# Performance work log

Measured on AMD Instinct MI355X. Metric: run time of the kernel, lower is better.

## Reference

```python
import jax, jax.numpy as jnp
import numpy as np

B = 2048      # query positions
N_OBS = 2048  # observed star positions
P = 15        # poly features = (d_max+1)(d_max+2)/2, d_max=4
G = 21        # graph features
E = 64        # n_graph_elems (columns of graph_dic)
D = 256       # opd_dim


def setup_inputs() -> dict:
    key = jax.random.key(0)
    k1, k2, k3, k4, k5, k6 = jax.random.split(key, 6)
    positions = jax.random.uniform(k1, (B, 2), dtype=jnp.float32)
    obs_pos = jax.random.uniform(k2, (N_OBS, 2), dtype=jnp.float32)
    poly_dic = jax.random.normal(k3, (N_OBS, P), dtype=jnp.float32)
    graph_dic = jax.random.normal(k4, (N_OBS, E), dtype=jnp.float32)
    alpha_poly = jnp.eye(P, dtype=jnp.float32)
    alpha_graph = jnp.eye(E, G, dtype=jnp.float32)
    S_poly = jax.random.uniform(k5, (P, D, D), minval=-0.001, maxval=0.001, dtype=jnp.float32)
    S_graph = jax.random.uniform(k6, (G, D, D), minval=-0.001, maxval=0.001, dtype=jnp.float32)
    return {"positions": positions, "obs_pos": obs_pos, "poly_dic": poly_dic,
            "graph_dic": graph_dic, "alpha_poly": alpha_poly, "alpha_graph": alpha_graph,
            "S_poly": S_poly, "S_graph": S_graph}


def reference(positions, obs_pos, poly_dic, graph_dic, alpha_poly, alpha_graph, S_poly, S_graph):
    # Brute-force 1-NN: [B, N_obs] squared distances, argmin over obs axis.
    d2 = jnp.sum((positions[:, None, :] - obs_pos[None, :, :]) ** 2, axis=-1)
    indices = jnp.argmin(d2, axis=1)                    # [B] int
    # Gather dictionary rows, mix with small alpha matrices.
    a_poly = poly_dic[indices] @ alpha_poly             # [B, P]
    a_graph = graph_dic[indices] @ alpha_graph          # [B, G]
    # Small-rank expansion into dense OPD maps.
    opd = (jnp.einsum('bp,pij->bij', a_poly, S_poly)
           + jnp.einsum('bg,gij->bij', a_graph, S_graph))  # [B, D, D]
    return opd
```

## Files before the change

kernel.cpp:

```cpp
#include <hip/hip_runtime.h>

#define NB 2048
#define NOBS 2048
#define NP 15
#define NG 21
#define NE 64
#define ND 256
#define NK 36
#define NDD (ND*ND)
#define RB 16
#define CT 4

typedef float vfloat4 __attribute__((ext_vector_type(4)));

__global__ __launch_bounds__(256) void knn_coeff_kernel(
    const float* __restrict__ positions,
    const float* __restrict__ obs_pos,
    const float* __restrict__ poly_dic,
    const float* __restrict__ graph_dic,
    const float* __restrict__ alpha_poly,
    const float* __restrict__ alpha_graph,
    float* __restrict__ coeffT)
{
    __shared__ float2 sobs[NOBS];
    __shared__ float  sd[256];
    __shared__ int    si[256];
    __shared__ int    sidx;

    const int tid = threadIdx.x;
    const int b   = blockIdx.x;

    const float2* obs2 = (const float2*)obs_pos;
    for (int i = tid; i < NOBS; i += 256) sobs[i] = obs2[i];

    const float qx = positions[2*b + 0];
    const float qy = positions[2*b + 1];
    __syncthreads();

    float bestd = 3.4e38f;
    int   besti = 0;
    #pragma unroll
    for (int it = 0; it < NOBS/256; ++it) {
        const int i = tid + it*256;
        const float dx = qx - sobs[i].x;
        const float dy = qy - sobs[i].y;
        const float d2 = dx*dx + dy*dy;
        if (d2 < bestd) { bestd = d2; besti = i; }
    }
    sd[tid] = bestd; si[tid] = besti;
    __syncthreads();

    for (int s = 128; s > 0; s >>= 1) {
        if (tid < s) {
            const float d2 = sd[tid + s];
            const int   i2 = si[tid + s];
            if (d2 < sd[tid] || (d2 == sd[tid] && i2 < si[tid])) {
                sd[tid] = d2; si[tid] = i2;
            }
        }
        __syncthreads();
    }
    if (tid == 0) sidx = si[0];
    __syncthreads();
    const int idx = sidx;

    if (tid < NP) {
        float acc = 0.f;
        #pragma unroll
        for (int q = 0; q < NP; ++q)
            acc += poly_dic[idx*NP + q] * alpha_poly[q*NP + tid];
        coeffT[(size_t)tid*NB + b] = acc;
    } else if (tid < NK) {
        const int g = tid - NP;
        float acc = 0.f;
        #pragma unroll
        for (int e = 0; e < NE; ++e)
            acc += graph_dic[idx*NE + e] * alpha_graph[e*NG + g];
        coeffT[(size_t)tid*NB + b] = acc;
    }
}

__global__ __launch_bounds__(256) void expand_kernel(
    const float* __restrict__ coeffT,
    const float* __restrict__ S_poly,
    const float* __restrict__ S_graph,
    float* __restrict__ out)
{
    const int j  = (blockIdx.x * 256 + threadIdx.x) * CT;
    const int b0 = blockIdx.y * RB;

    float acc[RB][CT];
    #pragma unroll
    for (int r = 0; r < RB; ++r)
        #pragma unroll
        for (int c = 0; c < CT; ++c)
            acc[r][c] = 0.f;

    #pragma unroll 2
    for (int k = 0; k < NP; ++k) {
        const vfloat4 sv = *(const vfloat4*)(S_poly + (size_t)k*NDD + j);
        const float*  cr = coeffT + (size_t)k*NB + b0;
        float cv[RB];
        *(vfloat4*)&cv[0]  = *(const vfloat4*)(cr + 0);
        *(vfloat4*)&cv[4]  = *(const vfloat4*)(cr + 4);
        *(vfloat4*)&cv[8]  = *(const vfloat4*)(cr + 8);
        *(vfloat4*)&cv[12] = *(const vfloat4*)(cr + 12);
        #pragma unroll
        for (int r = 0; r < RB; ++r)
            #pragma unroll
            for (int c = 0; c < CT; ++c)
                acc[r][c] += cv[r] * sv[c];
    }

    #pragma unroll 2
    for (int k = 0; k < NG; ++k) {
        const vfloat4 sv = *(const vfloat4*)(S_graph + (size_t)k*NDD + j);
        const float*  cr = coeffT + (size_t)(NP + k)*NB + b0;
        float cv[RB];
        *(vfloat4*)&cv[0]  = *(const vfloat4*)(cr + 0);
        *(vfloat4*)&cv[4]  = *(const vfloat4*)(cr + 4);
        *(vfloat4*)&cv[8]  = *(const vfloat4*)(cr + 8);
        *(vfloat4*)&cv[12] = *(const vfloat4*)(cr + 12);
        #pragma unroll
        for (int r = 0; r < RB; ++r)
            #pragma unroll
            for (int c = 0; c < CT; ++c)
                acc[r][c] += cv[r] * sv[c];
    }

    #pragma unroll
    for (int r = 0; r < RB; ++r) {
        vfloat4 v;
        v.x = acc[r][0]; v.y = acc[r][1]; v.z = acc[r][2]; v.w = acc[r][3];
        __builtin_nontemporal_store(
            v, (vfloat4*)(out + (size_t)(b0 + r)*NDD + j));
    }
}

extern "C" void kernel_launch(void* const* d_in, const int* in_sizes, int n_in,
                              void* d_out, int out_size, void* d_ws, size_t ws_size,
                              hipStream_t stream) {
    const float* positions   = (const float*)d_in[0];
    const float* obs_pos     = (const float*)d_in[1];
    const float* poly_dic    = (const float*)d_in[2];
    const float* graph_dic   = (const float*)d_in[3];
    const float* alpha_poly  = (const float*)d_in[4];
    const float* alpha_graph = (const float*)d_in[5];
    const float* S_poly      = (const float*)d_in[6];
    const float* S_graph     = (const float*)d_in[7];
    float* out = (float*)d_out;

    float* coeffT = (float*)d_ws;

    knn_coeff_kernel<<<NB, 256, 0, stream>>>(
        positions, obs_pos, poly_dic, graph_dic, alpha_poly, alpha_graph, coeffT);

    dim3 grid2(NDD/(256*CT), NB/RB);
    expand_kernel<<<grid2, 256, 0, stream>>>(coeffT, S_poly, S_graph, out);
}
```

Baseline: 613.4 us.

## Batch 8 queries per kNN block with shuffle argmin; merge expand loops with prefetch

```diff
diff --git a/kernel.cpp b/kernel.cpp
--- a/kernel.cpp
+++ b/kernel.cpp
@@ -10,6 +10,7 @@
 #define NDD (ND*ND)
 #define RB 16
 #define CT 4
+#define QB 8
 
 typedef float vfloat4 __attribute__((ext_vector_type(4)));
 
@@ -23,60 +24,63 @@
     float* __restrict__ coeffT)
 {
     __shared__ float2 sobs[NOBS];
-    __shared__ float  sd[256];
-    __shared__ int    si[256];
-    __shared__ int    sidx;
+    __shared__ float  sap[NP*NP];
+    __shared__ float  sag[NE*NG];
+    __shared__ int    sbest[QB];
 
     const int tid = threadIdx.x;
-    const int b   = blockIdx.x;
 
     const float2* obs2 = (const float2*)obs_pos;
     for (int i = tid; i < NOBS; i += 256) sobs[i] = obs2[i];
-
-    const float qx = positions[2*b + 0];
-    const float qy = positions[2*b + 1];
+    for (int i = tid; i < NP*NP; i += 256) sap[i] = alpha_poly[i];
+    for (int i = tid; i < NE*NG; i += 256) sag[i] = alpha_graph[i];
     __syncthreads();
 
-    float bestd = 3.4e38f;
-    int   besti = 0;
-    #pragma unroll
-    for (int it = 0; it < NOBS/256; ++it) {
-        const int i = tid + it*256;
+    const int w    = tid >> 6;
+    const int lane = tid & 63;
+    const int half = lane >> 5;
+    const int l32  = lane & 31;
+    const int q    = blockIdx.x * QB + 2*w + half;
+
+    const float qx = positions[2*q + 0];
+    const float qy = positions[2*q + 1];
+
+    unsigned long long best = ~0ull;
+    #pragma unroll 8
+    for (int it = 0; it < NOBS/32; ++it) {
+        const int i = l32 + it*32;
         const float dx = qx - sobs[i].x;
         const float dy = qy - sobs[i].y;
         const float d2 = dx*dx + dy*dy;
-        if (d2 < bestd) { bestd = d2; besti = i; }
+        const unsigned long long key =
+            ((unsigned long long)__float_as_uint(d2) << 32) | (unsigned)i;
+        if (key < best) best = key;
     }
-    sd[tid] = bestd; si[tid] = besti;
+    #pragma unroll
+    for (int m = 16; m > 0; m >>= 1) {
+        const unsigned long long o = __shfl_xor(best, m, 32);
+        if (o < best) best = o;
+    }
+    if (l32 == 0) sbest[2*w + half] = (int)(best & 0xffffffffu);
     __syncthreads();
 
-    for (int s = 128; s > 0; s >>= 1) {
-        if (tid < s) {
-            const float d2 = sd[tid + s];
-            const int   i2 = si[tid + s];
-            if (d2 < sd[tid] || (d2 == sd[tid] && i2 < si[tid])) {
-                sd[tid] = d2; si[tid] = i2;
-            }
+    for (int t = tid; t < QB*NK; t += 256) {
+        const int qq  = t / NK;
+        const int k   = t - qq*NK;
+        const int idx = sbest[qq];
+        const int b   = blockIdx.x * QB + qq;
+        float acc = 0.f;
+        if (k < NP) {
+            #pragma unroll
+            for (int p = 0; p < NP; ++p)
+                acc += poly_dic[idx*NP + p] * sap[p*NP + k];
+        } else {
+            const int g = k - NP;
+            #pragma unroll
+            for (int e = 0; e < NE; ++e)
+                acc += graph_dic[idx*NE + e] * sag[e*NG + g];
         }
-        __syncthreads();
-    }
-    if (tid == 0) sidx = si[0];
-    __syncthreads();
-    const int idx = sidx;
-
-    if (tid < NP) {
-        float acc = 0.f;
-        #pragma unroll
-        for (int q = 0; q < NP; ++q)
-            acc += poly_dic[idx*NP + q] * alpha_poly[q*NP + tid];
-        coeffT[(size_t)tid*NB + b] = acc;
-    } else if (tid < NK) {
-        const int g = tid - NP;
-        float acc = 0.f;
-        #pragma unroll
-        for (int e = 0; e < NE; ++e)
-            acc += graph_dic[idx*NE + e] * alpha_graph[e*NG + g];
-        coeffT[(size_t)tid*NB + b] = acc;
+        coeffT[(size_t)k*NB + b] = acc;
     }
 }
 
@@ -89,51 +93,44 @@
     const int j  = (blockIdx.x * 256 + threadIdx.x) * CT;
     const int b0 = blockIdx.y * RB;
 
-    float acc[RB][CT];
+    const float* __restrict__ sp = S_poly  + j;
+    const float* __restrict__ sg = S_graph + j;
+    const float* __restrict__ cb = coeffT + b0;
+
+    vfloat4 acc[RB];
     #pragma unroll
-    for (int r = 0; r < RB; ++r)
+    for (int r = 0; r < RB; ++r) acc[r] = (vfloat4)0.f;
+
+    vfloat4 sv = *(const vfloat4*)sp;
+    #pragma unroll
+    for (int k = 0; k < NK; ++k) {
+        vfloat4 svn = sv;
+        if (k + 1 < NK) {
+            const float* nsrc = (k + 1 < NP)
+                ? (sp + (size_t)(k + 1) * NDD)
+                : (sg + (size_t)(k + 1 - NP) * NDD);
+            svn = *(const vfloat4*)nsrc;
+        }
+        const float* cr = cb + (size_t)k * NB;
+        vfloat4 c0 = *(const vfloat4*)(cr + 0);
+        vfloat4 c1 = *(const vfloat4*)(cr + 4);
+        vfloat4 c2 = *(const vfloat4*)(cr + 8);
+        vfloat4 c3 = *(const vfloat4*)(cr + 12);
         #pragma unroll
-        for (int c = 0; c < CT; ++c)
-            acc[r][c] = 0.f;
-
-    #pragma unroll 2
-    for (int k = 0; k < NP; ++k) {
-        const vfloat4 sv = *(const vfloat4*)(S_poly + (size_t)k*NDD + j);
-        const float*  cr = coeffT + (size_t)k*NB + b0;
-        float cv[RB];
-        *(vfloat4*)&cv[0]  = *(const vfloat4*)(cr + 0);
-        *(vfloat4*)&cv[4]  = *(const vfloat4*)(cr + 4);
-        *(vfloat4*)&cv[8]  = *(const vfloat4*)(cr + 8);
-        *(vfloat4*)&cv[12] = *(const vfloat4*)(cr + 12);
+        for (int r = 0; r < 4; ++r) acc[r     ] += c0[r] * sv;
         #pragma unroll
-        for (int r = 0; r < RB; ++r)
-            #pragma unroll
-            for (int c = 0; c < CT; ++c)
-                acc[r][c] += cv[r] * sv[c];
-    }
-
-    #pragma unroll 2
-    for (int k = 0; k < NG; ++k) {
-        const vfloat4 sv = *(const vfloat4*)(S_graph + (size_t)k*NDD + j);
-        const float*  cr = coeffT + (size_t)(NP + k)*NB + b0;
-        float cv[RB];
-        *(vfloat4*)&cv[0]  = *(const vfloat4*)(cr + 0);
-        *(vfloat4*)&cv[4]  = *(const vfloat4*)(cr + 4);
-        *(vfloat4*)&cv[8]  = *(const vfloat4*)(cr + 8);
-        *(vfloat4*)&cv[12] = *(const vfloat4*)(cr + 12);
+        for (int r = 0; r < 4; ++r) acc[r + 4 ] += c1[r] * sv;
         #pragma unroll
-        for (int r = 0; r < RB; ++r)
-            #pragma unroll
-            for (int c = 0; c < CT; ++c)
-                acc[r][c] += cv[r] * sv[c];
+        for (int r = 0; r < 4; ++r) acc[r + 8 ] += c2[r] * sv;
+        #pragma unroll
+        for (int r = 0; r < 4; ++r) acc[r + 12] += c3[r] * sv;
+        sv = svn;
     }
 
     #pragma unroll
     for (int r = 0; r < RB; ++r) {
-        vfloat4 v;
-        v.x = acc[r][0]; v.y = acc[r][1]; v.z = acc[r][2]; v.w = acc[r][3];
         __builtin_nontemporal_store(
-            v, (vfloat4*)(out + (size_t)(b0 + r)*NDD + j));
+            acc[r], (vfloat4*)(out + (size_t)(b0 + r)*NDD + j));
     }
 }
 
@@ -152,7 +149,7 @@
 
     float* coeffT = (float*)d_ws;
 
-    knn_coeff_kernel<<<NB, 256, 0, stream>>>(
+    knn_coeff_kernel<<<NB/QB, 256, 0, stream>>>(
         positions, obs_pos, poly_dic, graph_dic, alpha_poly, alpha_graph, coeffT);
 
     dim3 grid2(NDD/(256*CT), NB/RB);
```

Result: faster. 575.3 us (-6.2%).
